# Kernel optimization log

Measured on AMD Instinct MI355X. Metric: run time of the kernel, lower is better.

The kernel has to match this reference:

```python
import jax, jax.numpy as jnp
import numpy as np

N, E, G = 50000, 300000, 256
H, LAT, VOCAB = 256, 64, 100
BN_EPS = 1e-5


def _bn(x, gamma, beta):
    # BatchNorm1d in training mode: per-feature batch mean / biased var
    mu = x.mean(axis=0)
    var = x.var(axis=0)
    return gamma * (x - mu) * jax.lax.rsqrt(var + BN_EPS) + beta


def _gconv(x, edge_attr, src, dst):
    # message: softplus(x_j + e), aggregate: scatter-add to dst, update: +(1+eps)*x with eps=0
    m = jax.nn.softplus(x[src] + edge_attr)          # [E, H]
    agg = jax.ops.segment_sum(m, dst, num_segments=N)  # [N, H]
    return agg + x


def setup_inputs() -> dict:
    key = jax.random.key(0)
    ks = jax.random.split(key, 16)
    inp = {
        "node_type": jax.random.randint(ks[0], (N,), 0, VOCAB),
        "edge_type": jax.random.randint(ks[1], (E,), 0, VOCAB),
        "edge_index": jax.random.randint(ks[2], (2, E), 0, N),
        "batch": jnp.sort(jax.random.randint(ks[3], (N,), 0, G)),
        "node_emb_w": jax.random.normal(ks[4], (VOCAB, H), jnp.float32),
        "edge_emb_w": jax.random.normal(ks[5], (VOCAB, H), jnp.float32),
        "g1": jnp.ones((H,), jnp.float32), "b1": jnp.zeros((H,), jnp.float32),
        "g2": jnp.ones((H,), jnp.float32), "b2": jnp.zeros((H,), jnp.float32),
        "g3": jnp.ones((H,), jnp.float32), "b3": jnp.zeros((H,), jnp.float32),
        "go1": jnp.ones((H,), jnp.float32), "bo1": jnp.zeros((H,), jnp.float32),
        "go2": jnp.ones((H // 2,), jnp.float32), "bo2": jnp.zeros((H // 2,), jnp.float32),
        "W1": jax.random.normal(ks[6], (2 * H, H), jnp.float32) * (2 * H) ** -0.5,
        "B1": jnp.zeros((H,), jnp.float32),
        "W2": jax.random.normal(ks[7], (H, H // 2), jnp.float32) * H ** -0.5,
        "B2": jnp.zeros((H // 2,), jnp.float32),
        "W3": jax.random.normal(ks[8], (H // 2, 2 * LAT), jnp.float32) * (H // 2) ** -0.5,
        "B3": jnp.zeros((2 * LAT,), jnp.float32),
    }
    return inp


def reference(node_type, edge_type, edge_index, batch,
              node_emb_w, edge_emb_w,
              g1, b1, g2, b2, g3, b3, go1, bo1, go2, bo2,
              W1, B1, W2, B2, W3, B3):
    act = jax.nn.softplus
    src, dst = edge_index[0], edge_index[1]
    h = node_emb_w[node_type]            # [N, H]
    e = edge_emb_w[edge_type]            # [E, H]
    h = act(_bn(_gconv(h, e, src, dst), g1, b1))
    h = act(_bn(_gconv(h, e, src, dst), g2, b2))
    h = _bn(_gconv(h, e, src, dst), g3, b3)
    h_global = jax.ops.segment_sum(h, batch, num_segments=G)  # [G, H]
    feat = jnp.concatenate([h, h_global[batch]], axis=-1)     # [N, 2H]
    feat = act(_bn(feat @ W1 + B1, go1, bo1))
    feat = act(_bn(feat @ W2 + B2, go2, bo2))
    out = feat @ W3 + B3                                      # [N, 2*LAT]
    return out[:, :LAT], out[:, LAT:]
```

## Files before the change

### kernel.cpp

```cpp
#include <hip/hip_runtime.h>
#include <hip/hip_bf16.h>

namespace {

constexpr int N = 50000;
constexpr int E = 300000;
constexpr int G = 256;
constexpr int H = 256;
constexpr float EPS = 1e-5f;
constexpr int NB = (N + 255) / 256;
constexpr int POOL_S = 16;
constexpr int GB = 1280;
constexpr float LOG2E = 1.4426950408889634f;
constexpr float LN2   = 0.6931471805599453f;

typedef unsigned short u16;
typedef __attribute__((ext_vector_type(8))) short bf16x8;
typedef __attribute__((ext_vector_type(4))) float f32x4;

__device__ __forceinline__ float expnabs(float z){
  float r; asm("v_exp_f32 %0, -abs(%1)" : "=v"(r) : "v"(z)); return r;
}
__device__ __forceinline__ float log2f_(float x){
  float r; asm("v_log_f32 %0, %1" : "=v"(r) : "v"(x)); return r;
}
__device__ __forceinline__ float spw(float zs){
  return fmaxf(zs, 0.f) + log2f_(1.f + expnabs(zs));
}
__device__ __forceinline__ u16 f2b(float f){
  union { float f; unsigned u; } v; v.f = f;
  unsigned r = v.u + 0x7FFF + ((v.u >> 16) & 1);
  return (u16)(r >> 16);
}
__device__ __forceinline__ float b2f(u16 u){
  union { unsigned i; float f; } v; v.i = ((unsigned)u) << 16; return v.f;
}
__device__ __forceinline__ float4 b2f4(ushort4 u){
  return make_float4(b2f(u.x), b2f(u.y), b2f(u.z), b2f(u.w));
}
__device__ __forceinline__ ushort4 f2b4(float4 v){
  ushort4 o; o.x = f2b(v.x); o.y = f2b(v.y); o.z = f2b(v.z); o.w = f2b(v.w);
  return o;
}

__global__ void k_pre(const int* __restrict__ nt, const float* __restrict__ nemb,
                      u16* __restrict__ xb, const int* __restrict__ dst,
                      int* __restrict__ cnt,
                      const float* __restrict__ W1, const float* __restrict__ W2,
                      const float* __restrict__ W3, const float* __restrict__ eemb,
                      u16* __restrict__ Wt1, u16* __restrict__ Wt2,
                      u16* __restrict__ Wt3, float* __restrict__ eembF){
  int idx = blockIdx.x * 256 + threadIdx.x;
  if (idx < N * 64){
    int i = idx >> 6, fq = (idx & 63) << 2;
    float4 v = *(const float4*)(nemb + (size_t)nt[i] * H + fq);
    v.x *= LOG2E; v.y *= LOG2E; v.z *= LOG2E; v.w *= LOG2E;
    *(ushort4*)(xb + (size_t)i * H + fq) = f2b4(v);
    return;
  }
  int j = idx - N * 64;
  if (j < E){ atomicAdd(&cnt[dst[j]], 1); return; }
  j -= E;
  if (j < 65536){ int c = j >> 8, k = j & 255; Wt1[j] = f2b(W1[(size_t)k * 256 + c]); return; }
  j -= 65536;
  if (j < 32768){ int c = j >> 8, k = j & 255; Wt2[j] = f2b(W2[(size_t)k * 128 + c]); return; }
  j -= 32768;
  if (j < 16384){ int c = j >> 7, k = j & 127; Wt3[j] = f2b(W3[(size_t)k * 128 + c]); return; }
  j -= 16384;
  if (j < 25600) eembF[j] = eemb[j] * LOG2E;
}

__global__ void k_scan1(const int* __restrict__ cnt, int* __restrict__ bsum){
  __shared__ int s[256];
  int t = threadIdx.x;
  int i = blockIdx.x * 256 + t;
  s[t] = (i < N) ? cnt[i] : 0;
  __syncthreads();
  for (int d = 128; d > 0; d >>= 1){
    if (t < d) s[t] += s[t + d];
    __syncthreads();
  }
  if (t == 0) bsum[blockIdx.x] = s[0];
}

__global__ void k_scan2(const int* __restrict__ bsum, int* __restrict__ bbase){
  __shared__ int s[256];
  int t = threadIdx.x;
  int orig = (t < NB) ? bsum[t] : 0;
  s[t] = orig;
  __syncthreads();
  for (int d = 1; d < 256; d <<= 1){
    int v = (t >= d) ? s[t - d] : 0;
    __syncthreads();
    s[t] += v;
    __syncthreads();
  }
  bbase[t] = s[t] - orig;
}

__global__ void k_scan3(const int* __restrict__ cnt, const int* __restrict__ bbase,
                        int* __restrict__ off, int* __restrict__ cur){
  __shared__ int s[256];
  int t = threadIdx.x;
  int i = blockIdx.x * 256 + t;
  int v = (i < N) ? cnt[i] : 0;
  s[t] = v;
  __syncthreads();
  for (int d = 1; d < 256; d <<= 1){
    int u = (t >= d) ? s[t - d] : 0;
    __syncthreads();
    s[t] += u;
    __syncthreads();
  }
  int excl = bbase[blockIdx.x] + s[t] - v;
  if (i < N){ off[i] = excl; cur[i] = excl; }
  if (i == N - 1) off[N] = excl + v;
}

__global__ void k_fill(const int* __restrict__ src, const int* __restrict__ dst,
                       const int* __restrict__ et, int* __restrict__ cur,
                       int2* __restrict__ edges_s){
  int e = blockIdx.x * 256 + threadIdx.x;
  if (e >= E) return;
  int d = dst[e];
  int p = atomicAdd(&cur[d], 1);
  edges_s[p] = make_int2(src[e] << 9, et[e] << 10);
}

__device__ __forceinline__ void acc_w(float4& acc, const float4 xs, const float4 es){
  acc.x += spw(xs.x + es.x);
  acc.y += spw(xs.y + es.y);
  acc.z += spw(xs.z + es.z);
  acc.w += spw(xs.w + es.w);
}

__global__ void k_gather(const u16* __restrict__ xb, u16* __restrict__ agg,
                         const int2* __restrict__ edges_s, const int* __restrict__ off,
                         const float* __restrict__ eembF,
                         float* __restrict__ sums, float* __restrict__ sumsq){
  __shared__ float reds[256][4];
  __shared__ float reds2[256][4];
  int tid = threadIdx.x;
  int w = tid >> 6, lane = tid & 63;
  int fx = lane << 3, fe = lane << 4;
  const char* xB = (const char*)xb;
  const char* eB = (const char*)eembF;
  float4 ls = make_float4(0.f, 0.f, 0.f, 0.f);
  float4 ls2 = make_float4(0.f, 0.f, 0.f, 0.f);
  for (int vb = blockIdx.x; vb < N / 4; vb += GB){
    int i = vb * 4 + w;
    float4 acc = b2f4(*(const ushort4*)(xB + ((size_t)i << 9) + fx));
    int lo = off[i], hi = off[i + 1];
    int j = lo;
    for (; j + 4 <= hi; j += 4){
      int2 s0 = edges_s[j + 0];
      int2 s1 = edges_s[j + 1];
      int2 s2 = edges_s[j + 2];
      int2 s3 = edges_s[j + 3];
      ushort4 x0 = *(const ushort4*)(xB + s0.x + fx);
      ushort4 x1 = *(const ushort4*)(xB + s1.x + fx);
      ushort4 x2 = *(const ushort4*)(xB + s2.x + fx);
      ushort4 x3 = *(const ushort4*)(xB + s3.x + fx);
      float4 e0 = *(const float4*)(eB + s0.y + fe);
      float4 e1 = *(const float4*)(eB + s1.y + fe);
      float4 e2 = *(const float4*)(eB + s2.y + fe);
      float4 e3 = *(const float4*)(eB + s3.y + fe);
      acc_w(acc, b2f4(x0), e0);
      acc_w(acc, b2f4(x1), e1);
      acc_w(acc, b2f4(x2), e2);
      acc_w(acc, b2f4(x3), e3);
    }
    if (j + 2 <= hi){
      int2 s0 = edges_s[j + 0];
      int2 s1 = edges_s[j + 1];
      ushort4 x0 = *(const ushort4*)(xB + s0.x + fx);
      ushort4 x1 = *(const ushort4*)(xB + s1.x + fx);
      float4 e0 = *(const float4*)(eB + s0.y + fe);
      float4 e1 = *(const float4*)(eB + s1.y + fe);
      acc_w(acc, b2f4(x0), e0);
      acc_w(acc, b2f4(x1), e1);
      j += 2;
    }
    if (j < hi){
      int2 s0 = edges_s[j];
      ushort4 x0 = *(const ushort4*)(xB + s0.x + fx);
      float4 e0 = *(const float4*)(eB + s0.y + fe);
      acc_w(acc, b2f4(x0), e0);
    }
    acc.x *= LN2; acc.y *= LN2; acc.z *= LN2; acc.w *= LN2;
    ls.x += acc.x; ls.y += acc.y; ls.z += acc.z; ls.w += acc.w;
    ls2.x += acc.x * acc.x; ls2.y += acc.y * acc.y;
    ls2.z += acc.z * acc.z; ls2.w += acc.w * acc.w;
    *(ushort4*)((char*)agg + ((size_t)i << 9) + fx) = f2b4(acc);
  }
  reds[tid][0] = ls.x;  reds[tid][1] = ls.y;  reds[tid][2] = ls.z;  reds[tid][3] = ls.w;
  reds2[tid][0] = ls2.x; reds2[tid][1] = ls2.y; reds2[tid][2] = ls2.z; reds2[tid][3] = ls2.w;
  __syncthreads();
  int f = tid;
  float ts = 0.f, ts2 = 0.f;
  #pragma unroll
  for (int w2 = 0; w2 < 4; ++w2){
    int s = w2 * 64 + (f >> 2);
    ts += reds[s][f & 3];
    ts2 += reds2[s][f & 3];
  }
  atomicAdd(&sums[f], ts);
  atomicAdd(&sumsq[f], ts2);
}

template<int ACT, int SCALED>
__global__ void k_norm(const u16* __restrict__ in, u16* __restrict__ outb,
                       const float* __restrict__ sums, const float* __restrict__ sumsq,
                       const float* __restrict__ gamma, const float* __restrict__ beta,
                       int n4, int fmask){
  int idx = blockIdx.x * 256 + threadIdx.x;
  if (idx >= n4) return;
  int base = idx << 2;
  int f = base & fmask;
  float4 s = *(const float4*)(sums + f);
  float4 q = *(const float4*)(sumsq + f);
  float4 g = *(const float4*)(gamma + f);
  float4 bt = *(const float4*)(beta + f);
  float4 v = b2f4(*(const ushort4*)(in + base));
  const float inv = 1.f / N;
  float m, var, a, c;
  m = s.x * inv; var = q.x * inv - m * m; a = g.x * rsqrtf(var + EPS); c = bt.x - m * a; v.x = a * v.x + c;
  m = s.y * inv; var = q.y * inv - m * m; a = g.y * rsqrtf(var + EPS); c = bt.y - m * a; v.y = a * v.y + c;
  m = s.z * inv; var = q.z * inv - m * m; a = g.z * rsqrtf(var + EPS); c = bt.z - m * a; v.z = a * v.z + c;
  m = s.w * inv; var = q.w * inv - m * m; a = g.w * rsqrtf(var + EPS); c = bt.w - m * a; v.w = a * v.w + c;
  if (ACT){
    v.x = spw(v.x * LOG2E); v.y = spw(v.y * LOG2E);
    v.z = spw(v.z * LOG2E); v.w = spw(v.w * LOG2E);
    if (!SCALED){ v.x *= LN2; v.y *= LN2; v.z *= LN2; v.w *= LN2; }
  }
  *(ushort4*)(outb + base) = f2b4(v);
}

__global__ void k_pool_seg(const u16* __restrict__ xb, const int* __restrict__ batch,
                           float* __restrict__ hg){
  int g = blockIdx.x, sl = blockIdx.y;
  int f = threadIdx.x;
  int lo = 0, hi = N;
  while (lo < hi){ int m = (lo + hi) >> 1; if (batch[m] < g) lo = m + 1; else hi = m; }
  int start = lo;
  lo = 0; hi = N;
  while (lo < hi){ int m = (lo + hi) >> 1; if (batch[m] < g + 1) lo = m + 1; else hi = m; }
  int end = lo;
  int len = end - start;
  int a = start + (int)((long)len * sl / POOL_S);
  int b = start + (int)((long)len * (sl + 1) / POOL_S);
  if (a >= b) return;
  float s = 0.f;
  for (int i = a; i < b; ++i) s += b2f(xb[(size_t)i * H + f]);
  atomicAdd(&hg[g * H + f], s);
}

__global__ void k_hgw(const float* __restrict__ hg, const float* __restrict__ W1,
                      const float* __restrict__ B1, float* __restrict__ hgW){
  int g = blockIdx.x, c = threadIdx.x;
  float acc = B1[c];
  for (int k = 0; k < H; ++k)
    acc += hg[g * H + k] * W1[(size_t)(H + k) * H + c];
  hgW[g * H + c] = acc;
}

template<int K, int NC, int MODE, int WR, int STATS>
__global__ void k_mgemm(const u16* __restrict__ Ab, const u16* __restrict__ Wt,
                        const float* __restrict__ epi, const int* __restrict__ batch,
                        u16* __restrict__ outb, float* __restrict__ outf,
                        float* __restrict__ sums, float* __restrict__ sumsq){
  __shared__ float reds[256][4];
  __shared__ float reds2[256][4];
  constexpr int WC = 4 / WR;
  int tid = threadIdx.x;
  int w = tid >> 6, lane = tid & 63;
  int quad = lane >> 4, l15 = lane & 15;
  int wr = w / WC, wc = w % WC;
  int rowBase = blockIdx.x * (WR * 64) + wr * 64;
  int colBase = wc * 64;
  const u16* arow[4];
  #pragma unroll
  for (int t = 0; t < 4; ++t){
    int am = rowBase + t * 16 + l15;
    if (am >= N) am = N - 1;
    arow[t] = Ab + (size_t)am * K + quad * 8;
  }
  const u16* brow[4];
  #pragma unroll
  for (int u = 0; u < 4; ++u)
    brow[u] = Wt + (size_t)(colBase + u * 16 + l15) * K + quad * 8;
  f32x4 acc[4][4] = {};
  for (int k0 = 0; k0 < K; k0 += 32){
    bf16x8 a[4], b[4];
    #pragma unroll
    for (int t = 0; t < 4; ++t) a[t] = *(const bf16x8*)(arow[t] + k0);
    #pragma unroll
    for (int u = 0; u < 4; ++u) b[u] = *(const bf16x8*)(brow[u] + k0);
    #pragma unroll
    for (int t = 0; t < 4; ++t)
      #pragma unroll
      for (int u = 0; u < 4; ++u)
        acc[t][u] = __builtin_amdgcn_mfma_f32_16x16x32_bf16(a[t], b[u], acc[t][u], 0, 0, 0);
  }
  float ls[4] = {0.f, 0.f, 0.f, 0.f};
  float ls2[4] = {0.f, 0.f, 0.f, 0.f};
  #pragma unroll
  for (int t = 0; t < 4; ++t){
    #pragma unroll
    for (int r = 0; r < 4; ++r){
      int row = rowBase + t * 16 + quad * 4 + r;
      if (row >= N) continue;
      int g = (MODE == 0) ? batch[row] : 0;
      #pragma unroll
      for (int u = 0; u < 4; ++u){
        int n = colBase + u * 16 + l15;
        float v = acc[t][u][r];
        if (MODE == 0){
          v += epi[(size_t)g * NC + n];
          outb[(size_t)row * NC + n] = f2b(v);
        } else if (MODE == 1){
          v += epi[n];
          outb[(size_t)row * NC + n] = f2b(v);
        } else {
          v += epi[n];
          if (n < 64) outf[(size_t)row * 64 + n] = v;
          else        outf[(size_t)N * 64 + (size_t)row * 64 + (n - 64)] = v;
        }
        if (STATS){ ls[u] += v; ls2[u] += v * v; }
      }
    }
  }
  if (STATS){
    #pragma unroll
    for (int u = 0; u < 4; ++u){ reds[tid][u] = ls[u]; reds2[tid][u] = ls2[u]; }
    __syncthreads();
    int f = tid;
    if (f < NC){
      int fl = f & 15, fu = (f >> 4) & 3, fw = f >> 6;
      float ts = 0.f, ts2 = 0.f;
      if (WR == 1){
        #pragma unroll
        for (int q = 0; q < 4; ++q){
          int s = fw * 64 + q * 16 + fl;
          ts += reds[s][fu]; ts2 += reds2[s][fu];
        }
      } else {
        #pragma unroll
        for (int r2 = 0; r2 < 2; ++r2)
          #pragma unroll
          for (int q = 0; q < 4; ++q){
            int s = (r2 * 2 + fw) * 64 + q * 16 + fl;
            ts += reds[s][fu]; ts2 += reds2[s][fu];
          }
      }
      atomicAdd(&sums[f], ts);
      atomicAdd(&sumsq[f], ts2);
    }
  }
}

}

extern "C" void kernel_launch(void* const* d_in, const int* in_sizes, int n_in,
                              void* d_out, int out_size, void* d_ws, size_t ws_size,
                              hipStream_t stream){
  const int* node_type = (const int*)d_in[0];
  const int* edge_type = (const int*)d_in[1];
  const int* src       = (const int*)d_in[2];
  const int* dst       = src + E;
  const int* batch     = (const int*)d_in[3];
  const float* nemb = (const float*)d_in[4];
  const float* eemb = (const float*)d_in[5];
  const float* gs[3] = {(const float*)d_in[6], (const float*)d_in[8], (const float*)d_in[10]};
  const float* bs[3] = {(const float*)d_in[7], (const float*)d_in[9], (const float*)d_in[11]};
  const float* go1 = (const float*)d_in[12]; const float* bo1 = (const float*)d_in[13];
  const float* go2 = (const float*)d_in[14]; const float* bo2 = (const float*)d_in[15];
  const float* W1 = (const float*)d_in[16]; const float* B1 = (const float*)d_in[17];
  const float* W2 = (const float*)d_in[18]; const float* B2 = (const float*)d_in[19];
  const float* W3 = (const float*)d_in[20]; const float* B3 = (const float*)d_in[21];
  float* outf = (float*)d_out;

  char* p = (char*)d_ws;
  int*   cnt    = (int*)p;              p += (size_t)N * 4;
  float* hg     = (float*)p;            p += (size_t)G * H * 4;
  float* statsA = (float*)p;            p += 5 * 512 * 4;
  size_t zeroBytes = (size_t)p - (size_t)d_ws;
  float* hgW    = (float*)p;            p += (size_t)G * H * 4;
  int*   off    = (int*)p;              p += (size_t)(N + 1) * 4;
  int*   cur    = (int*)p;              p += (size_t)N * 4;
  int*   bsum   = (int*)p;              p += 256 * 4;
  int*   bbase  = (int*)p;              p += 256 * 4;
  int2*  edges_s= (int2*)p;             p += (size_t)E * 8;
  u16*   xb     = (u16*)p;              p += (size_t)N * H * 2;
  u16*   agg    = (u16*)p;              p += (size_t)N * H * 2;
  u16*   xf     = (u16*)p;              p += (size_t)N * 128 * 2;
  u16*   Wt1    = (u16*)p;              p += 65536 * 2;
  u16*   Wt2    = (u16*)p;              p += 32768 * 2;
  u16*   Wt3    = (u16*)p;              p += 16384 * 2;
  float* eembF  = (float*)p;            p += 25600 * 4;
  float* sumsL[5], *sumsqL[5];
  for (int k = 0; k < 5; ++k){ sumsL[k] = statsA + k * 512; sumsqL[k] = statsA + k * 512 + 256; }

  hipMemsetAsync(d_ws, 0, zeroBytes, stream);

  const int preItems = N * 64 + E + 65536 + 32768 + 16384 + 25600;
  k_pre<<<(preItems + 255) / 256, 256, 0, stream>>>(
      node_type, nemb, xb, dst, cnt, W1, W2, W3, eemb, Wt1, Wt2, Wt3, eembF);
  k_scan1<<<NB, 256, 0, stream>>>(cnt, bsum);
  k_scan2<<<1, 256, 0, stream>>>(bsum, bbase);
  k_scan3<<<NB, 256, 0, stream>>>(cnt, bbase, off, cur);
  k_fill<<<(E + 255) / 256, 256, 0, stream>>>(src, dst, edge_type, cur, edges_s);

  for (int l = 0; l < 3; ++l){
    k_gather<<<GB, 256, 0, stream>>>(xb, agg, edges_s, off, eembF, sumsL[l], sumsqL[l]);
    if (l < 2)
      k_norm<1, 1><<<(N * 64 + 255) / 256, 256, 0, stream>>>(
          agg, xb, sumsL[l], sumsqL[l], gs[l], bs[l], N * 64, 255);
    else
      k_norm<0, 0><<<(N * 64 + 255) / 256, 256, 0, stream>>>(
          agg, xb, sumsL[l], sumsqL[l], gs[l], bs[l], N * 64, 255);
  }

  {
    dim3 pg(G, POOL_S);
    k_pool_seg<<<pg, H, 0, stream>>>(xb, batch, hg);
  }
  k_hgw<<<G, H, 0, stream>>>(hg, W1, B1, hgW);

  k_mgemm<256, 256, 0, 1, 1><<<(N + 63) / 64, 256, 0, stream>>>(
      xb, Wt1, hgW, batch, agg, nullptr, sumsL[3], sumsqL[3]);
  k_norm<1, 0><<<(N * 64 + 255) / 256, 256, 0, stream>>>(
      agg, xb, sumsL[3], sumsqL[3], go1, bo1, N * 64, 255);

  k_mgemm<256, 128, 1, 2, 1><<<(N + 127) / 128, 256, 0, stream>>>(
      xb, Wt2, B2, nullptr, xf, nullptr, sumsL[4], sumsqL[4]);
  k_norm<1, 0><<<(N * 32 + 255) / 256, 256, 0, stream>>>(
      xf, xb, sumsL[4], sumsqL[4], go2, bo2, N * 32, 127);

  k_mgemm<128, 128, 2, 2, 0><<<(N + 127) / 128, 256, 0, stream>>>(
      xb, Wt3, B3, nullptr, nullptr, outf, nullptr, nullptr);
}
```

Measured before the change: 532.7 us.

## Stage edge embedding table in LDS with 1024-thread gather blocks

Each gather block first copies the full fp32 edge-embedding table (100 KB) into shared memory, then reads per-edge embeddings from LDS instead of global memory. To amortise that copy, blocks grow from 256 to 1024 threads, and the grid shrinks to 256 blocks with 16 nodes per iteration. The large LDS footprint allows only one block per CU, which caps occupancy and limits latency hiding for the random feature gathers. It also adds a 100 KB per-block preload in every layer.

Result: faster. 481.3 us (-9.6%).

```diff
diff --git a/kernel.cpp b/kernel.cpp
--- a/kernel.cpp
+++ b/kernel.cpp
@@ -10,7 +10,8 @@
 constexpr float EPS = 1e-5f;
 constexpr int NB = (N + 255) / 256;
 constexpr int POOL_S = 16;
-constexpr int GB = 1280;
+constexpr int GBL = 256;
+constexpr int NVB = N / 16;
 constexpr float LOG2E = 1.4426950408889634f;
 constexpr float LN2   = 0.6931471805599453f;
 
@@ -134,21 +135,31 @@
   acc.w += spw(xs.w + es.w);
 }
 
-__global__ void k_gather(const u16* __restrict__ xb, u16* __restrict__ agg,
-                         const int2* __restrict__ edges_s, const int* __restrict__ off,
-                         const float* __restrict__ eembF,
-                         float* __restrict__ sums, float* __restrict__ sumsq){
-  __shared__ float reds[256][4];
-  __shared__ float reds2[256][4];
+__global__ __launch_bounds__(1024)
+void k_gather(const u16* __restrict__ xb, u16* __restrict__ agg,
+              const int2* __restrict__ edges_s, const int* __restrict__ off,
+              const float* __restrict__ eembF,
+              float* __restrict__ sums, float* __restrict__ sumsq){
+  __shared__ __align__(16) float elds[25600];
+  __shared__ float reds[1024][4];
+  __shared__ float reds2[1024][4];
   int tid = threadIdx.x;
   int w = tid >> 6, lane = tid & 63;
   int fx = lane << 3, fe = lane << 4;
   const char* xB = (const char*)xb;
-  const char* eB = (const char*)eembF;
+  const char* eL = (const char*)elds;
+
+  {
+    const float4* s4 = (const float4*)eembF;
+    float4* d4 = (float4*)elds;
+    for (int t = tid; t < 6400; t += 1024) d4[t] = s4[t];
+  }
+  __syncthreads();
+
   float4 ls = make_float4(0.f, 0.f, 0.f, 0.f);
   float4 ls2 = make_float4(0.f, 0.f, 0.f, 0.f);
-  for (int vb = blockIdx.x; vb < N / 4; vb += GB){
-    int i = vb * 4 + w;
+  for (int vb = blockIdx.x; vb < NVB; vb += GBL){
+    int i = vb * 16 + w;
     float4 acc = b2f4(*(const ushort4*)(xB + ((size_t)i << 9) + fx));
     int lo = off[i], hi = off[i + 1];
     int j = lo;
@@ -161,10 +172,10 @@
       ushort4 x1 = *(const ushort4*)(xB + s1.x + fx);
       ushort4 x2 = *(const ushort4*)(xB + s2.x + fx);
       ushort4 x3 = *(const ushort4*)(xB + s3.x + fx);
-      float4 e0 = *(const float4*)(eB + s0.y + fe);
-      float4 e1 = *(const float4*)(eB + s1.y + fe);
-      float4 e2 = *(const float4*)(eB + s2.y + fe);
-      float4 e3 = *(const float4*)(eB + s3.y + fe);
+      float4 e0 = *(const float4*)(eL + s0.y + fe);
+      float4 e1 = *(const float4*)(eL + s1.y + fe);
+      float4 e2 = *(const float4*)(eL + s2.y + fe);
+      float4 e3 = *(const float4*)(eL + s3.y + fe);
       acc_w(acc, b2f4(x0), e0);
       acc_w(acc, b2f4(x1), e1);
       acc_w(acc, b2f4(x2), e2);
@@ -175,8 +186,8 @@
       int2 s1 = edges_s[j + 1];
       ushort4 x0 = *(const ushort4*)(xB + s0.x + fx);
       ushort4 x1 = *(const ushort4*)(xB + s1.x + fx);
-      float4 e0 = *(const float4*)(eB + s0.y + fe);
-      float4 e1 = *(const float4*)(eB + s1.y + fe);
+      float4 e0 = *(const float4*)(eL + s0.y + fe);
+      float4 e1 = *(const float4*)(eL + s1.y + fe);
       acc_w(acc, b2f4(x0), e0);
       acc_w(acc, b2f4(x1), e1);
       j += 2;
@@ -184,7 +195,7 @@
     if (j < hi){
       int2 s0 = edges_s[j];
       ushort4 x0 = *(const ushort4*)(xB + s0.x + fx);
-      float4 e0 = *(const float4*)(eB + s0.y + fe);
+      float4 e0 = *(const float4*)(eL + s0.y + fe);
       acc_w(acc, b2f4(x0), e0);
     }
     acc.x *= LN2; acc.y *= LN2; acc.z *= LN2; acc.w *= LN2;
@@ -196,16 +207,18 @@
   reds[tid][0] = ls.x;  reds[tid][1] = ls.y;  reds[tid][2] = ls.z;  reds[tid][3] = ls.w;
   reds2[tid][0] = ls2.x; reds2[tid][1] = ls2.y; reds2[tid][2] = ls2.z; reds2[tid][3] = ls2.w;
   __syncthreads();
-  int f = tid;
-  float ts = 0.f, ts2 = 0.f;
-  #pragma unroll
-  for (int w2 = 0; w2 < 4; ++w2){
-    int s = w2 * 64 + (f >> 2);
-    ts += reds[s][f & 3];
-    ts2 += reds2[s][f & 3];
-  }
-  atomicAdd(&sums[f], ts);
-  atomicAdd(&sumsq[f], ts2);
+  if (tid < 256){
+    int f = tid;
+    float ts = 0.f, ts2 = 0.f;
+    #pragma unroll
+    for (int w2 = 0; w2 < 16; ++w2){
+      int s = w2 * 64 + (f >> 2);
+      ts += reds[s][f & 3];
+      ts2 += reds2[s][f & 3];
+    }
+    atomicAdd(&sums[f], ts);
+    atomicAdd(&sumsq[f], ts2);
+  }
 }
 
 template<int ACT, int SCALED>
@@ -412,7 +425,7 @@
   k_fill<<<(E + 255) / 256, 256, 0, stream>>>(src, dst, edge_type, cur, edges_s);
 
   for (int l = 0; l < 3; ++l){
-    k_gather<<<GB, 256, 0, stream>>>(xb, agg, edges_s, off, eembF, sumsL[l], sumsqL[l]);
+    k_gather<<<GBL, 1024, 0, stream>>>(xb, agg, edges_s, off, eembF, sumsL[l], sumsqL[l]);
     if (l < 2)
       k_norm<1, 1><<<(N * 64 + 255) / 256, 256, 0, stream>>>(
           agg, xb, sumsL[l], sumsqL[l], gs[l], bs[l], N * 64, 255);
```
